# Performance work log

Measured on AMD Instinct MI355X. Metric: run time of the kernel, lower is better.

## Reference

```python
import jax, jax.numpy as jnp
import numpy as np
from jax import lax

DN = ('NHWC', 'HWIO', 'NHWC')


def setup_inputs() -> dict:
    key = jax.random.key(0)
    k1, k2, k3, k4, k5, k6 = jax.random.split(key, 6)
    B = 1024
    vals = jax.random.normal(k1, (B, 64, 64, 1), dtype=jnp.float32)
    active = (jax.random.uniform(k2, (B, 64, 64, 1)) < 0.1).astype(jnp.float32)
    x = vals * active
    W1 = jax.random.normal(k3, (3, 3, 1, 64), dtype=jnp.float32) * 0.1
    b1 = jax.random.normal(k4, (64,), dtype=jnp.float32) * 0.1
    W2 = jax.random.normal(k5, (3, 3, 64, 32), dtype=jnp.float32) * 0.05
    b2 = jax.random.normal(k6, (32,), dtype=jnp.float32) * 0.05
    return {"x": x, "W1": W1, "b1": b1, "W2": W2, "b2": b2}


def reference(x, W1, b1, W2, b2):
    # x: [B, 64, 64, 1] NHWC (spconv from_dense layout); active sites = nonzero pixels
    m0 = (jnp.abs(x).max(axis=-1, keepdims=True) > 0).astype(x.dtype)  # [B,64,64,1]
    # SparseConv2d(1,64,3,stride=1, pad=0): output indices = any active input in 3x3 window
    m1 = lax.reduce_window(m0, jnp.array(0, x.dtype), lax.max,
                           (1, 3, 3, 1), (1, 1, 1, 1), 'VALID')  # [B,62,62,1]
    y = lax.conv_general_dilated(x, W1, (1, 1), 'VALID', dimension_numbers=DN)
    y = (y + b1) * m1  # bias only at active output sites; [B,62,62,64]
    # SparseInverseConv2d(64,32,3): transposed conv restricted to the ORIGINAL
    # active index set (indice_key='cp0'), i.e. output only where m0 is active.
    z = lax.conv_transpose(y, W2, (1, 1), 'VALID', dimension_numbers=DN)  # [B,64,64,32]
    z = (z + b2) * m0
    # SparseConvTensor.dense() returns NCHW
    return jnp.transpose(z, (0, 3, 1, 2))
```

## Files before the change

### kernel.cpp

```cpp
#include <hip/hip_runtime.h>

#define BDIM 256
#define KC_STRIDE 28
#define CASE_STRIDE (32 * KC_STRIDE)
#define SP 2052

typedef float floatx4 __attribute__((ext_vector_type(4)));

__device__ __forceinline__ int casef(int p) {
  return ((unsigned)(p - 2) < 60u) ? 2 : (p < 2 ? p : p - 59);
}

__device__ __forceinline__ unsigned long long spread4(unsigned x) {
  unsigned long long v = x & 0xFFFFull;
  v = (v | (v << 24)) & 0x000000FF000000FFull;
  v = (v | (v << 12)) & 0x000F000F000F000Full;
  v = (v | (v << 6))  & 0x0303030303030303ull;
  v = (v | (v << 3))  & 0x1111111111111111ull;
  return v;
}

__global__ __launch_bounds__(BDIM) void prep_kernel(
    const float* __restrict__ W1, const float* __restrict__ b1,
    const float* __restrict__ W2, const float* __restrict__ b2,
    float* __restrict__ ws) {
  __shared__ float Mlds[9 * 9 * 32];
  __shared__ float BvL[9 * 32];
  const int tid = threadIdx.x;
  const int co = tid & 31;
  for (int tap = tid >> 5; tap < 9; tap += 8) {
    float acc[9] = {0.f, 0.f, 0.f, 0.f, 0.f, 0.f, 0.f, 0.f, 0.f};
    float accB = 0.f;
    for (int ci = 0; ci < 64; ++ci) {
      float w2 = W2[(tap * 64 + ci) * 32 + co];
      accB = fmaf(b1[ci], w2, accB);
#pragma unroll
      for (int e = 0; e < 9; ++e) acc[e] = fmaf(W1[e * 64 + ci], w2, acc[e]);
    }
#pragma unroll
    for (int e = 0; e < 9; ++e) Mlds[(tap * 9 + e) * 32 + co] = acc[e];
    BvL[tap * 32 + co] = accB;
  }
  __syncthreads();

  const int a = blockIdx.x / 5, c = blockIdx.x % 5;
  const int dmask[5] = {4, 6, 7, 3, 1};
  const int Da = dmask[a], Dc = dmask[c];
  for (int t = tid; t < CASE_STRIDE; t += BDIM) {
    int cc = t / KC_STRIDE, r = t % KC_STRIDE;
    float s = 0.f;
    if (r < 25) {
      int u = r / 5, v = r % 5;
      for (int di = 0; di < 3; ++di) {
        if (!((Da >> di) & 1)) continue;
        int ei = u - di;
        if ((unsigned)ei > 2u) continue;
        for (int dj = 0; dj < 3; ++dj) {
          if (!((Dc >> dj) & 1)) continue;
          int ej = v - dj;
          if ((unsigned)ej > 2u) continue;
          s += Mlds[((di * 3 + dj) * 9 + ei * 3 + ej) * 32 + cc];
        }
      }
    } else if (r == 25) {
      s = b2[cc];
      for (int di = 0; di < 3; ++di)
        if ((Da >> di) & 1)
          for (int dj = 0; dj < 3; ++dj)
            if ((Dc >> dj) & 1) s += BvL[(di * 3 + dj) * 32 + cc];
    }
    ws[blockIdx.x * CASE_STRIDE + t] = s;
  }
}

__global__ __launch_bounds__(BDIM) void main_kernel(
    const float* __restrict__ x, const float* __restrict__ ws,
    float* __restrict__ out) {
  const int bb = blockIdx.x;
  const int b = bb >> 1;
  const int r0 = (bb & 1) << 5;
  const int tid = threadIdx.x;
  const int lane = tid & 63;
  const int wave = tid >> 6;

  __shared__ __align__(16) float xp[36 * 68];
  __shared__ __align__(16) float S[8][SP];
  __shared__ __align__(16) float KiL[CASE_STRIDE];
  __shared__ unsigned long long Rm[32];
  __shared__ unsigned short aqi[448], aqb[128];
  __shared__ int nqi_sh, nqb_sh;

  if (tid == 0) { nqi_sh = 0; nqb_sh = 0; }
  for (int i = tid; i < CASE_STRIDE; i += BDIM) KiL[i] = ws[12 * CASE_STRIDE + i];

  const float* xb = x + (size_t)b * 4096;

  if (tid < 144) {
    int i = tid >> 2, c = tid & 3;
    xp[i * 68 + ((c & 1) + ((c >> 1) * 66))] = 0.f;
  }
#pragma unroll
  for (int j = 0; j < 2; ++j) {
    int it = tid + (j << 8);
    int k = it >> 4;
    int q = it & 15;
    float4 v = *reinterpret_cast<const float4*>(xb + (r0 + k) * 64 + (q << 2));
    float2* d2 = reinterpret_cast<float2*>(&xp[(k + 2) * 68 + 2 + (q << 2)]);
    d2[0] = make_float2(v.x, v.y);
    d2[1] = make_float2(v.z, v.w);
    unsigned long long b0 = __ballot(v.x != 0.f);
    unsigned long long b1 = __ballot(v.y != 0.f);
    unsigned long long b2 = __ballot(v.z != 0.f);
    unsigned long long b3 = __ballot(v.w != 0.f);
    if ((lane & 15) == 0) {
      int rslice = lane >> 4;
      unsigned s0 = (unsigned)((b0 >> (rslice << 4)) & 0xFFFFu);
      unsigned s1 = (unsigned)((b1 >> (rslice << 4)) & 0xFFFFu);
      unsigned s2 = (unsigned)((b2 >> (rslice << 4)) & 0xFFFFu);
      unsigned s3 = (unsigned)((b3 >> (rslice << 4)) & 0xFFFFu);
      Rm[k] = spread4(s0) | (spread4(s1) << 1) | (spread4(s2) << 2) |
              (spread4(s3) << 3);
    }
  }
  if (tid < 64) {
    int sel = tid >> 4, q = tid & 15;
    int i = (sel < 2) ? sel : sel + 32;
    int r = r0 - 2 + i;
    float4 v = make_float4(0.f, 0.f, 0.f, 0.f);
    if ((unsigned)r < 64u)
      v = *reinterpret_cast<const float4*>(xb + r * 64 + (q << 2));
    float2* d2 = reinterpret_cast<float2*>(&xp[i * 68 + 2 + (q << 2)]);
    d2[0] = make_float2(v.x, v.y);
    d2[1] = make_float2(v.z, v.w);
  }
  __syncthreads();

  for (int g = tid; g < 512; g += BDIM) {
    int k = g >> 4, q0 = (g & 15) << 2;
    unsigned bits = (unsigned)(Rm[k] >> q0) & 0xFu;
    if (!bits) continue;
    int p = r0 + k;
    bool inter = ((unsigned)(p - 2) < 60u) && ((unsigned)(q0 - 4) <= 52u);
    if (inter) {
      aqi[atomicAdd(&nqi_sh, 1)] = (unsigned short)g;
    } else {
      aqb[atomicAdd(&nqb_sh, 1)] = (unsigned short)g;
    }
  }
  __syncthreads();

  const int nqi = nqi_sh, nqb = nqb_sh;
  float* outb = out + (size_t)b * (32 * 4096);
  const int co4 = tid & 3;

  for (int cg = 0; cg < 4; ++cg) {
    const int co_lo = (cg << 3) + co4;
    float KA[26], KB[26];
    {
      const float* KpA = &KiL[co_lo * KC_STRIDE];
      const float* KpB = &KiL[(co_lo + 4) * KC_STRIDE];
#pragma unroll
      for (int j = 0; j < 26; ++j) { KA[j] = KpA[j]; KB[j] = KpB[j]; }
    }
    for (int n = tid; n < nqi * 4; n += BDIM) {
      int g = aqi[n >> 2];
      int k = g >> 4, q0 = (g & 15) << 2;
      float ba = KA[25], bbv = KB[25];
      float a0 = ba, a1 = ba, a2 = ba, a3 = ba;
      float b0 = bbv, b1 = bbv, b2 = bbv, b3 = bbv;
#pragma unroll
      for (int u = 0; u < 5; ++u) {
        const float* xr = &xp[(k + u) * 68 + q0];
        float4 xa = *reinterpret_cast<const float4*>(xr);
        float4 xc = *reinterpret_cast<const float4*>(xr + 4);
        float xv[8] = {xa.x, xa.y, xa.z, xa.w, xc.x, xc.y, xc.z, xc.w};
#pragma unroll
        for (int v = 0; v < 5; ++v) {
          float ka = KA[u * 5 + v], kb = KB[u * 5 + v];
          a0 = fmaf(xv[v], ka, a0);
          a1 = fmaf(xv[v + 1], ka, a1);
          a2 = fmaf(xv[v + 2], ka, a2);
          a3 = fmaf(xv[v + 3], ka, a3);
          b0 = fmaf(xv[v], kb, b0);
          b1 = fmaf(xv[v + 1], kb, b1);
          b2 = fmaf(xv[v + 2], kb, b2);
          b3 = fmaf(xv[v + 3], kb, b3);
        }
      }
      int so = (k << 6) + q0;
      *reinterpret_cast<float4*>(&S[co4][so]) = make_float4(a0, a1, a2, a3);
      *reinterpret_cast<float4*>(&S[co4 + 4][so]) = make_float4(b0, b1, b2, b3);
    }
    for (int n = tid; n < nqb * 8; n += BDIM) {
      int g = aqb[n >> 3];
      int cs = n & 7;
      int co = (cg << 3) + cs;
      int k = g >> 4, q0 = (g & 15) << 2;
      int p = r0 + k;
      int cp = casef(p);
      const float* K0 = ws + ((cp * 5 + casef(q0)) * 32 + co) * KC_STRIDE;
      const float* K1 = ws + ((cp * 5 + casef(q0 + 1)) * 32 + co) * KC_STRIDE;
      const float* K2 = ws + ((cp * 5 + casef(q0 + 2)) * 32 + co) * KC_STRIDE;
      const float* K3 = ws + ((cp * 5 + casef(q0 + 3)) * 32 + co) * KC_STRIDE;
      float z0 = K0[25], z1 = K1[25], z2 = K2[25], z3 = K3[25];
#pragma unroll
      for (int u = 0; u < 5; ++u) {
        const float* xr = &xp[(k + u) * 68 + q0];
        float4 xa = *reinterpret_cast<const float4*>(xr);
        float4 xc = *reinterpret_cast<const float4*>(xr + 4);
        float xv[8] = {xa.x, xa.y, xa.z, xa.w, xc.x, xc.y, xc.z, xc.w};
#pragma unroll
        for (int v = 0; v < 5; ++v) {
          int o = u * 5 + v;
          z0 = fmaf(xv[v], K0[o], z0);
          z1 = fmaf(xv[v + 1], K1[o], z1);
          z2 = fmaf(xv[v + 2], K2[o], z2);
          z3 = fmaf(xv[v + 3], K3[o], z3);
        }
      }
      *reinterpret_cast<float4*>(&S[cs][(k << 6) + q0]) =
          make_float4(z0, z1, z2, z3);
    }
    asm volatile("s_waitcnt lgkmcnt(0)" ::: "memory");
    __builtin_amdgcn_s_barrier();
    {
      int co_a = (cg << 3) + wave;
      float* dstA = outb + (((size_t)co_a) << 12) + (r0 << 6);
      float* dstB = outb + (((size_t)(co_a + 4)) << 12) + (r0 << 6);
      const floatx4* SpA = reinterpret_cast<const floatx4*>(&S[wave][0]);
      const floatx4* SpB = reinterpret_cast<const floatx4*>(&S[wave + 4][0]);
#pragma unroll
      for (int i = 0; i < 8; ++i) {
        int f4 = (i << 6) + lane;
        int kk = f4 >> 4, q0 = (f4 & 15) << 2;
        unsigned bits = (unsigned)(Rm[kk] >> q0) & 0xFu;
        floatx4 va = SpA[f4];
        floatx4 vb = SpB[f4];
        if (!(bits & 1u)) { va.x = 0.f; vb.x = 0.f; }
        if (!(bits & 2u)) { va.y = 0.f; vb.y = 0.f; }
        if (!(bits & 4u)) { va.z = 0.f; vb.z = 0.f; }
        if (!(bits & 8u)) { va.w = 0.f; vb.w = 0.f; }
        __builtin_nontemporal_store(va, reinterpret_cast<floatx4*>(dstA + (f4 << 2)));
        __builtin_nontemporal_store(vb, reinterpret_cast<floatx4*>(dstB + (f4 << 2)));
      }
    }
    asm volatile("s_waitcnt lgkmcnt(0)" ::: "memory");
    __builtin_amdgcn_s_barrier();
  }
}

extern "C" void kernel_launch(void* const* d_in, const int* in_sizes, int n_in,
                              void* d_out, int out_size, void* d_ws, size_t ws_size,
                              hipStream_t stream) {
  const float* x  = (const float*)d_in[0];
  const float* W1 = (const float*)d_in[1];
  const float* b1 = (const float*)d_in[2];
  const float* W2 = (const float*)d_in[3];
  const float* b2 = (const float*)d_in[4];
  float* out = (float*)d_out;
  float* ws  = (float*)d_ws;
  int B = in_sizes[0] / 4096;

  hipLaunchKernelGGL(prep_kernel, dim3(25), dim3(BDIM), 0, stream, W1, b1, W2, b2, ws);
  hipLaunchKernelGGL(main_kernel, dim3(2 * B), dim3(BDIM), 0, stream, x, ws, out);
}
```

Measured before the change: 121.8 us.

## Process whole image per block with 512 threads instead of half-image blocks

Each block now handles a full 64x64 image with 512 threads, instead of two blocks of 256 threads each covering 32 rows. This drops the duplicated halo-row loads and the repeated per-block setup (kernel-table copy, mask building). Shared memory per block roughly doubles, and the grid halves to 1024 blocks, which may reduce occupancy and load balance. The store loop now has each wave write one channel over 16 iterations.

```diff
diff --git a/kernel.cpp b/kernel.cpp
--- a/kernel.cpp
+++ b/kernel.cpp
@@ -1,9 +1,10 @@
 #include <hip/hip_runtime.h>
 
-#define BDIM 256
+#define BDIM 512
+#define PDIM 256
 #define KC_STRIDE 28
 #define CASE_STRIDE (32 * KC_STRIDE)
-#define SP 2052
+#define SP 4100
 
 typedef float floatx4 __attribute__((ext_vector_type(4)));
 
@@ -20,7 +21,7 @@
   return v;
 }
 
-__global__ __launch_bounds__(BDIM) void prep_kernel(
+__global__ __launch_bounds__(PDIM) void prep_kernel(
     const float* __restrict__ W1, const float* __restrict__ b1,
     const float* __restrict__ W2, const float* __restrict__ b2,
     float* __restrict__ ws) {
@@ -46,7 +47,7 @@
   const int a = blockIdx.x / 5, c = blockIdx.x % 5;
   const int dmask[5] = {4, 6, 7, 3, 1};
   const int Da = dmask[a], Dc = dmask[c];
-  for (int t = tid; t < CASE_STRIDE; t += BDIM) {
+  for (int t = tid; t < CASE_STRIDE; t += PDIM) {
     int cc = t / KC_STRIDE, r = t % KC_STRIDE;
     float s = 0.f;
     if (r < 25) {
@@ -76,18 +77,16 @@
 __global__ __launch_bounds__(BDIM) void main_kernel(
     const float* __restrict__ x, const float* __restrict__ ws,
     float* __restrict__ out) {
-  const int bb = blockIdx.x;
-  const int b = bb >> 1;
-  const int r0 = (bb & 1) << 5;
+  const int b = blockIdx.x;
   const int tid = threadIdx.x;
   const int lane = tid & 63;
   const int wave = tid >> 6;
 
-  __shared__ __align__(16) float xp[36 * 68];
+  __shared__ __align__(16) float xp[68 * 68];
   __shared__ __align__(16) float S[8][SP];
   __shared__ __align__(16) float KiL[CASE_STRIDE];
-  __shared__ unsigned long long Rm[32];
-  __shared__ unsigned short aqi[448], aqb[128];
+  __shared__ unsigned long long Rm[64];
+  __shared__ unsigned short aqi[840], aqb[184];
   __shared__ int nqi_sh, nqb_sh;
 
   if (tid == 0) { nqi_sh = 0; nqb_sh = 0; }
@@ -95,16 +94,16 @@
 
   const float* xb = x + (size_t)b * 4096;
 
-  if (tid < 144) {
+  if (tid < 272) {
     int i = tid >> 2, c = tid & 3;
     xp[i * 68 + ((c & 1) + ((c >> 1) * 66))] = 0.f;
   }
 #pragma unroll
   for (int j = 0; j < 2; ++j) {
-    int it = tid + (j << 8);
+    int it = tid + (j << 9);
     int k = it >> 4;
     int q = it & 15;
-    float4 v = *reinterpret_cast<const float4*>(xb + (r0 + k) * 64 + (q << 2));
+    float4 v = *reinterpret_cast<const float4*>(xb + k * 64 + (q << 2));
     float2* d2 = reinterpret_cast<float2*>(&xp[(k + 2) * 68 + 2 + (q << 2)]);
     d2[0] = make_float2(v.x, v.y);
     d2[1] = make_float2(v.z, v.w);
@@ -124,22 +123,17 @@
   }
   if (tid < 64) {
     int sel = tid >> 4, q = tid & 15;
-    int i = (sel < 2) ? sel : sel + 32;
-    int r = r0 - 2 + i;
-    float4 v = make_float4(0.f, 0.f, 0.f, 0.f);
-    if ((unsigned)r < 64u)
-      v = *reinterpret_cast<const float4*>(xb + r * 64 + (q << 2));
+    int i = (sel < 2) ? sel : sel + 64;
     float2* d2 = reinterpret_cast<float2*>(&xp[i * 68 + 2 + (q << 2)]);
-    d2[0] = make_float2(v.x, v.y);
-    d2[1] = make_float2(v.z, v.w);
+    d2[0] = make_float2(0.f, 0.f);
+    d2[1] = make_float2(0.f, 0.f);
   }
   __syncthreads();
 
-  for (int g = tid; g < 512; g += BDIM) {
-    int k = g >> 4, q0 = (g & 15) << 2;
-    unsigned bits = (unsigned)(Rm[k] >> q0) & 0xFu;
+  for (int g = tid; g < 1024; g += BDIM) {
+    int p = g >> 4, q0 = (g & 15) << 2;
+    unsigned bits = (unsigned)(Rm[p] >> q0) & 0xFu;
     if (!bits) continue;
-    int p = r0 + k;
     bool inter = ((unsigned)(p - 2) < 60u) && ((unsigned)(q0 - 4) <= 52u);
     if (inter) {
       aqi[atomicAdd(&nqi_sh, 1)] = (unsigned short)g;
@@ -196,8 +190,7 @@
       int cs = n & 7;
       int co = (cg << 3) + cs;
       int k = g >> 4, q0 = (g & 15) << 2;
-      int p = r0 + k;
-      int cp = casef(p);
+      int cp = casef(k);
       const float* K0 = ws + ((cp * 5 + casef(q0)) * 32 + co) * KC_STRIDE;
       const float* K1 = ws + ((cp * 5 + casef(q0 + 1)) * 32 + co) * KC_STRIDE;
       const float* K2 = ws + ((cp * 5 + casef(q0 + 2)) * 32 + co) * KC_STRIDE;
@@ -224,24 +217,20 @@
     asm volatile("s_waitcnt lgkmcnt(0)" ::: "memory");
     __builtin_amdgcn_s_barrier();
     {
-      int co_a = (cg << 3) + wave;
-      float* dstA = outb + (((size_t)co_a) << 12) + (r0 << 6);
-      float* dstB = outb + (((size_t)(co_a + 4)) << 12) + (r0 << 6);
-      const floatx4* SpA = reinterpret_cast<const floatx4*>(&S[wave][0]);
-      const floatx4* SpB = reinterpret_cast<const floatx4*>(&S[wave + 4][0]);
-#pragma unroll
-      for (int i = 0; i < 8; ++i) {
+      int co_w = (cg << 3) + wave;
+      float* dst = outb + (((size_t)co_w) << 12);
+      const floatx4* Sp = reinterpret_cast<const floatx4*>(&S[wave][0]);
+#pragma unroll
+      for (int i = 0; i < 16; ++i) {
         int f4 = (i << 6) + lane;
         int kk = f4 >> 4, q0 = (f4 & 15) << 2;
         unsigned bits = (unsigned)(Rm[kk] >> q0) & 0xFu;
-        floatx4 va = SpA[f4];
-        floatx4 vb = SpB[f4];
-        if (!(bits & 1u)) { va.x = 0.f; vb.x = 0.f; }
-        if (!(bits & 2u)) { va.y = 0.f; vb.y = 0.f; }
-        if (!(bits & 4u)) { va.z = 0.f; vb.z = 0.f; }
-        if (!(bits & 8u)) { va.w = 0.f; vb.w = 0.f; }
-        __builtin_nontemporal_store(va, reinterpret_cast<floatx4*>(dstA + (f4 << 2)));
-        __builtin_nontemporal_store(vb, reinterpret_cast<floatx4*>(dstB + (f4 << 2)));
+        floatx4 v = Sp[f4];
+        if (!(bits & 1u)) v.x = 0.f;
+        if (!(bits & 2u)) v.y = 0.f;
+        if (!(bits & 4u)) v.z = 0.f;
+        if (!(bits & 8u)) v.w = 0.f;
+        __builtin_nontemporal_store(v, reinterpret_cast<floatx4*>(dst + (f4 << 2)));
       }
     }
     asm volatile("s_waitcnt lgkmcnt(0)" ::: "memory");
@@ -261,6 +250,6 @@
   float* ws  = (float*)d_ws;
   int B = in_sizes[0] / 4096;
 
-  hipLaunchKernelGGL(prep_kernel, dim3(25), dim3(BDIM), 0, stream, W1, b1, W2, b2, ws);
-  hipLaunchKernelGGL(main_kernel, dim3(2 * B), dim3(BDIM), 0, stream, x, ws, out);
-}
+  hipLaunchKernelGGL(prep_kernel, dim3(25), dim3(PDIM), 0, stream, W1, b1, W2, b2, ws);
+  hipLaunchKernelGGL(main_kernel, dim3(B), dim3(BDIM), 0, stream, x, ws, out);
+}
```

Result: slower. 125.3 us (+2.9%).

## Process 16 output channels per pass and load weights from global

Applied to the files above, without the earlier changes.

Doubles the shared staging buffer so each block handles 16 output channels per pass, halving the channel-group loop and its barriers. Interior weights are now read directly from global memory instead of a shared copy, and each wave stores four channel planes. The larger shared footprint likely cuts resident blocks per CU, reducing latency hiding.

```diff
diff --git a/kernel.cpp b/kernel.cpp
--- a/kernel.cpp
+++ b/kernel.cpp
@@ -84,14 +84,12 @@
   const int wave = tid >> 6;
 
   __shared__ __align__(16) float xp[36 * 68];
-  __shared__ __align__(16) float S[8][SP];
-  __shared__ __align__(16) float KiL[CASE_STRIDE];
+  __shared__ __align__(16) float S[16][SP];
   __shared__ unsigned long long Rm[32];
   __shared__ unsigned short aqi[448], aqb[128];
   __shared__ int nqi_sh, nqb_sh;
 
   if (tid == 0) { nqi_sh = 0; nqb_sh = 0; }
-  for (int i = tid; i < CASE_STRIDE; i += BDIM) KiL[i] = ws[12 * CASE_STRIDE + i];
 
   const float* xb = x + (size_t)b * 4096;
 
@@ -151,19 +149,20 @@
 
   const int nqi = nqi_sh, nqb = nqb_sh;
   float* outb = out + (size_t)b * (32 * 4096);
-  const int co4 = tid & 3;
-
-  for (int cg = 0; cg < 4; ++cg) {
-    const int co_lo = (cg << 3) + co4;
+  const float* wsKi = ws + 12 * CASE_STRIDE;
+  const int cs = tid & 7;
+
+  for (int sg = 0; sg < 2; ++sg) {
+    const int c_lo = (sg << 4) + cs;
     float KA[26], KB[26];
     {
-      const float* KpA = &KiL[co_lo * KC_STRIDE];
-      const float* KpB = &KiL[(co_lo + 4) * KC_STRIDE];
+      const float* KpA = wsKi + c_lo * KC_STRIDE;
+      const float* KpB = wsKi + (c_lo + 8) * KC_STRIDE;
 #pragma unroll
       for (int j = 0; j < 26; ++j) { KA[j] = KpA[j]; KB[j] = KpB[j]; }
     }
-    for (int n = tid; n < nqi * 4; n += BDIM) {
-      int g = aqi[n >> 2];
+    for (int n = tid; n < nqi * 8; n += BDIM) {
+      int g = aqi[n >> 3];
       int k = g >> 4, q0 = (g & 15) << 2;
       float ba = KA[25], bbv = KB[25];
       float a0 = ba, a1 = ba, a2 = ba, a3 = ba;
@@ -188,13 +187,13 @@
         }
       }
       int so = (k << 6) + q0;
-      *reinterpret_cast<float4*>(&S[co4][so]) = make_float4(a0, a1, a2, a3);
-      *reinterpret_cast<float4*>(&S[co4 + 4][so]) = make_float4(b0, b1, b2, b3);
-    }
-    for (int n = tid; n < nqb * 8; n += BDIM) {
-      int g = aqb[n >> 3];
-      int cs = n & 7;
-      int co = (cg << 3) + cs;
+      *reinterpret_cast<float4*>(&S[cs][so]) = make_float4(a0, a1, a2, a3);
+      *reinterpret_cast<float4*>(&S[cs + 8][so]) = make_float4(b0, b1, b2, b3);
+    }
+    for (int n = tid; n < nqb * 16; n += BDIM) {
+      int g = aqb[n >> 4];
+      int cs16 = n & 15;
+      int co = (sg << 4) + cs16;
       int k = g >> 4, q0 = (g & 15) << 2;
       int p = r0 + k;
       int cp = casef(p);
@@ -218,30 +217,30 @@
           z3 = fmaf(xv[v + 3], K3[o], z3);
         }
       }
-      *reinterpret_cast<float4*>(&S[cs][(k << 6) + q0]) =
+      *reinterpret_cast<float4*>(&S[cs16][(k << 6) + q0]) =
           make_float4(z0, z1, z2, z3);
     }
     asm volatile("s_waitcnt lgkmcnt(0)" ::: "memory");
     __builtin_amdgcn_s_barrier();
     {
-      int co_a = (cg << 3) + wave;
-      float* dstA = outb + (((size_t)co_a) << 12) + (r0 << 6);
-      float* dstB = outb + (((size_t)(co_a + 4)) << 12) + (r0 << 6);
-      const floatx4* SpA = reinterpret_cast<const floatx4*>(&S[wave][0]);
-      const floatx4* SpB = reinterpret_cast<const floatx4*>(&S[wave + 4][0]);
-#pragma unroll
-      for (int i = 0; i < 8; ++i) {
-        int f4 = (i << 6) + lane;
-        int kk = f4 >> 4, q0 = (f4 & 15) << 2;
-        unsigned bits = (unsigned)(Rm[kk] >> q0) & 0xFu;
-        floatx4 va = SpA[f4];
-        floatx4 vb = SpB[f4];
-        if (!(bits & 1u)) { va.x = 0.f; vb.x = 0.f; }
-        if (!(bits & 2u)) { va.y = 0.f; vb.y = 0.f; }
-        if (!(bits & 4u)) { va.z = 0.f; vb.z = 0.f; }
-        if (!(bits & 8u)) { va.w = 0.f; vb.w = 0.f; }
-        __builtin_nontemporal_store(va, reinterpret_cast<floatx4*>(dstA + (f4 << 2)));
-        __builtin_nontemporal_store(vb, reinterpret_cast<floatx4*>(dstB + (f4 << 2)));
+      int pl0 = wave << 2;
+#pragma unroll
+      for (int pl = 0; pl < 4; ++pl) {
+        int co = (sg << 4) + pl0 + pl;
+        float* dst = outb + (((size_t)co) << 12) + (r0 << 6);
+        const floatx4* Sp = reinterpret_cast<const floatx4*>(&S[pl0 + pl][0]);
+#pragma unroll
+        for (int i = 0; i < 8; ++i) {
+          int f4 = (i << 6) + lane;
+          int kk = f4 >> 4, q0 = (f4 & 15) << 2;
+          unsigned bits = (unsigned)(Rm[kk] >> q0) & 0xFu;
+          floatx4 v = Sp[f4];
+          if (!(bits & 1u)) v.x = 0.f;
+          if (!(bits & 2u)) v.y = 0.f;
+          if (!(bits & 4u)) v.z = 0.f;
+          if (!(bits & 8u)) v.w = 0.f;
+          __builtin_nontemporal_store(v, reinterpret_cast<floatx4*>(dst + (f4 << 2)));
+        }
       }
     }
     asm volatile("s_waitcnt lgkmcnt(0)" ::: "memory");
```

Result: slower. 149.4 us (+22.7%).
